# Optimization experiments

Measured on AMD Instinct MI355X. Metric: run time of the kernel, lower is better.

The kernel has to match this reference:

```python
import jax, jax.numpy as jnp
import numpy as np

B, T, D = 64, 2048, 256

def setup_inputs() -> dict:
    key = jax.random.key(0)
    k1, _ = jax.random.split(key)
    ts = jnp.arange(T, dtype=jnp.float32) * 0.01  # increasing time grid
    noise = jax.random.normal(k1, (B, T, D), dtype=jnp.float32)
    mu = jnp.zeros((D,), jnp.float32)
    log_kappa = jnp.full((D,), -0.7, jnp.float32)
    log_sigma = jnp.full((D,), -0.7, jnp.float32)
    return {"ts": ts, "noise": noise, "mu": mu, "log_kappa": log_kappa, "log_sigma": log_sigma}

def _A_Q(kappa, sigma, dt):
    # exact OU transition coefficients; dt: [T-1,1], kappa/sigma: [D] -> [T-1,D]
    A = jnp.exp(-kappa * dt)
    two_k_dt = 2.0 * kappa * dt
    small = (two_k_dt < 1e-6).astype(dt.dtype)
    Q_exact = sigma ** 2 * (1.0 - jnp.exp(-two_k_dt)) / jnp.maximum(2.0 * kappa, 1e-12)
    Q_taylor = sigma ** 2 * dt * (1.0 - kappa * dt + two_k_dt ** 2 / 6.0)
    Q = small * Q_taylor + (1.0 - small) * Q_exact
    return A, Q

def reference(ts, noise, mu, log_kappa, log_sigma):
    kappa = jax.nn.softplus(log_kappa) + 1e-6
    sigma = jax.nn.softplus(log_sigma) + 1e-6
    var0 = sigma ** 2 / (2.0 * kappa)                      # stationary variance [D]
    y0 = mu + noise[:, 0, :] * jnp.sqrt(var0)              # [B,D]
    dt = jnp.maximum(ts[1:] - ts[:-1], 1e-6)[:, None]      # [T-1,1]
    A, Q = _A_Q(kappa, sigma, dt)                          # [T-1,D]
    # mean = mu + A*(y-mu) = A*y + mu*(1-A); fold noise in ahead of the scan
    b = mu * (1.0 - A)                                     # [T-1,D]
    eps = jnp.swapaxes(noise[:, 1:, :], 0, 1) * jnp.sqrt(Q)[:, None, :]  # [T-1,B,D]

    def step(y, xs):
        A_k, b_k, e_k = xs
        y_new = A_k * y + b_k + e_k
        return y_new, y_new

    _, ys = jax.lax.scan(step, y0, (A, b, eps))            # [T-1,B,D]
    y = jnp.concatenate([y0[None], ys], axis=0)            # [T,B,D]
    return jnp.swapaxes(y, 0, 1)                           # [B,T,D]
```

## Files before the change

### kernel.cpp

```cpp
#include <hip/hip_runtime.h>
#include <math.h>

#define BB 64
#define TT 2048
#define DD 256
#define DP 128
#define SS 32
#define LL (TT / SS)


__device__ __forceinline__ float softplus_f(float x) {
    return (x > 0.f) ? (x + log1pf(expf(-x))) : log1pf(expf(x));
}

struct OUParams {
    float kx, ky;
    float s2x, s2y;
    float rx, ry;
    float mx, my;
};

__device__ __forceinline__ OUParams load_params(const float2* __restrict__ mu2,
                                                const float2* __restrict__ lk2,
                                                const float2* __restrict__ ls2,
                                                int tid) {
    float2 lk = lk2[tid], ls = ls2[tid], mu = mu2[tid];
    OUParams p;
    p.kx = softplus_f(lk.x) + 1e-6f;
    p.ky = softplus_f(lk.y) + 1e-6f;
    float sx = softplus_f(ls.x) + 1e-6f;
    float sy = softplus_f(ls.y) + 1e-6f;
    p.s2x = sx * sx;
    p.s2y = sy * sy;
    p.rx = p.s2x / fmaxf(2.f * p.kx, 1e-12f);
    p.ry = p.s2y / fmaxf(2.f * p.ky, 1e-12f);
    p.mx = mu.x;
    p.my = mu.y;
    return p;
}

__device__ __forceinline__ void ou_coeff(float dt, float kappa, float s2, float r,
                                         float mu, float& A, float& bm, float& sQ) {
    float e = kappa * dt;
    A = __expf(-e);
    float two = 2.f * e;
    float Qe = r * (1.f - A * A);
    float Qt = s2 * dt * fmaf(two * two, (1.f / 6.f), 1.f - e);
    float Q = (two < 1e-6f) ? Qt : Qe;
    sQ = sqrtf(Q);
    bm = mu * (1.f - A);
}

__global__ __launch_bounds__(128) void ou_pass1(
    const float* __restrict__ ts, const float2* __restrict__ noise2,
    const float2* __restrict__ mu2, const float2* __restrict__ lk2,
    const float2* __restrict__ ls2,
    float2* __restrict__ Pw, float2* __restrict__ Uw) {
    __shared__ float dts[LL];
    const int tid = threadIdx.x;
    const int s = blockIdx.x / BB;
    const int b = blockIdx.x % BB;
    const int t0 = s * LL;

    if (tid < LL) {
        int k = t0 + tid;
        float dt = 1e-6f;
        if (k >= 1) dt = fmaxf(ts[k] - ts[k - 1], 1e-6f);
        dts[tid] = dt;
    }
    __syncthreads();

    OUParams p = load_params(mu2, lk2, ls2, tid);
    const float2* np = noise2 + (size_t)b * TT * DP + tid;

    float2 U = {0.f, 0.f};
    float2 P = {1.f, 1.f};
    int kstart = t0;
    if (s == 0) {
        float2 n0 = np[0];
        U.x = fmaf(n0.x, sqrtf(p.rx), p.mx);
        U.y = fmaf(n0.y, sqrtf(p.ry), p.my);
        P.x = 0.f; P.y = 0.f;
        kstart = 1;
    }

#pragma unroll 4
    for (int k = kstart; k < t0 + LL; ++k) {
        float dt = dts[k - t0];
        float2 n = np[(size_t)k * DP];
        float Ax, bmx, sqx, Ay, bmy, sqy;
        ou_coeff(dt, p.kx, p.s2x, p.rx, p.mx, Ax, bmx, sqx);
        ou_coeff(dt, p.ky, p.s2y, p.ry, p.my, Ay, bmy, sqy);
        float cx = fmaf(sqx, n.x, bmx);
        float cy = fmaf(sqy, n.y, bmy);
        U.x = fmaf(Ax, U.x, cx);
        U.y = fmaf(Ay, U.y, cy);
        P.x *= Ax;
        P.y *= Ay;
    }

    size_t idx = ((size_t)s * BB + b) * DP + tid;
    Pw[idx] = P;
    Uw[idx] = U;
}

__global__ __launch_bounds__(128) void ou_pass2(
    const float2* __restrict__ Pw, const float2* __restrict__ Uw,
    float2* __restrict__ Ys) {
    const int tid = threadIdx.x;
    const int b = blockIdx.x;
    const size_t stride = (size_t)BB * DP;
    const size_t i0 = (size_t)b * DP + tid;

    float2 inc = Uw[i0];
    for (int s = 1; s < SS; ++s) {
        size_t idx = i0 + (size_t)s * stride;
        float2 Pv = Pw[idx];
        float2 Uv = Uw[idx];
        Ys[idx] = inc;
        inc.x = fmaf(Pv.x, inc.x, Uv.x);
        inc.y = fmaf(Pv.y, inc.y, Uv.y);
    }
}

__global__ __launch_bounds__(128) void ou_pass3(
    const float* __restrict__ ts, const float2* __restrict__ noise2,
    const float2* __restrict__ mu2, const float2* __restrict__ lk2,
    const float2* __restrict__ ls2,
    const float2* __restrict__ Ys, float2* __restrict__ out2) {
    __shared__ float dts[LL];
    const int tid = threadIdx.x;
    const int s = blockIdx.x / BB;
    const int b = blockIdx.x % BB;
    const int t0 = s * LL;

    if (tid < LL) {
        int k = t0 + tid;
        float dt = 1e-6f;
        if (k >= 1) dt = fmaxf(ts[k] - ts[k - 1], 1e-6f);
        dts[tid] = dt;
    }
    __syncthreads();

    OUParams p = load_params(mu2, lk2, ls2, tid);
    const float2* np = noise2 + (size_t)b * TT * DP + tid;
    float2* op = out2 + (size_t)b * TT * DP + tid;

    float2 y;
    int kstart = t0;
    if (s == 0) {
        float2 n0 = np[0];
        y.x = fmaf(n0.x, sqrtf(p.rx), p.mx);
        y.y = fmaf(n0.y, sqrtf(p.ry), p.my);
        op[0] = y;
        kstart = 1;
    } else {
        y = Ys[((size_t)s * BB + b) * DP + tid];
    }

#pragma unroll 4
    for (int k = kstart; k < t0 + LL; ++k) {
        float dt = dts[k - t0];
        float2 n = np[(size_t)k * DP];
        float Ax, bmx, sqx, Ay, bmy, sqy;
        ou_coeff(dt, p.kx, p.s2x, p.rx, p.mx, Ax, bmx, sqx);
        ou_coeff(dt, p.ky, p.s2y, p.ry, p.my, Ay, bmy, sqy);
        float cx = fmaf(sqx, n.x, bmx);
        float cy = fmaf(sqy, n.y, bmy);
        y.x = fmaf(Ax, y.x, cx);
        y.y = fmaf(Ay, y.y, cy);
        op[(size_t)k * DP] = y;
    }
}

__global__ __launch_bounds__(128) void ou_fallback(
    const float* __restrict__ ts, const float2* __restrict__ noise2,
    const float2* __restrict__ mu2, const float2* __restrict__ lk2,
    const float2* __restrict__ ls2, float2* __restrict__ out2) {
    __shared__ float dts[TT];
    const int tid = threadIdx.x;
    const int b = blockIdx.x;
    for (int i = tid; i < TT; i += 128) {
        float dt = 1e-6f;
        if (i >= 1) dt = fmaxf(ts[i] - ts[i - 1], 1e-6f);
        dts[i] = dt;
    }
    __syncthreads();

    OUParams p = load_params(mu2, lk2, ls2, tid);
    const float2* np = noise2 + (size_t)b * TT * DP + tid;
    float2* op = out2 + (size_t)b * TT * DP + tid;

    float2 n0 = np[0];
    float2 y;
    y.x = fmaf(n0.x, sqrtf(p.rx), p.mx);
    y.y = fmaf(n0.y, sqrtf(p.ry), p.my);
    op[0] = y;

#pragma unroll 4
    for (int k = 1; k < TT; ++k) {
        float dt = dts[k];
        float2 n = np[(size_t)k * DP];
        float Ax, bmx, sqx, Ay, bmy, sqy;
        ou_coeff(dt, p.kx, p.s2x, p.rx, p.mx, Ax, bmx, sqx);
        ou_coeff(dt, p.ky, p.s2y, p.ry, p.my, Ay, bmy, sqy);
        float cx = fmaf(sqx, n.x, bmx);
        float cy = fmaf(sqy, n.y, bmy);
        y.x = fmaf(Ax, y.x, cx);
        y.y = fmaf(Ay, y.y, cy);
        op[(size_t)k * DP] = y;
    }
}

extern "C" void kernel_launch(void* const* d_in, const int* in_sizes, int n_in,
                              void* d_out, int out_size, void* d_ws, size_t ws_size,
                              hipStream_t stream) {
    const float* ts = (const float*)d_in[0];
    const float2* noise2 = (const float2*)d_in[1];
    const float2* mu2 = (const float2*)d_in[2];
    const float2* lk2 = (const float2*)d_in[3];
    const float2* ls2 = (const float2*)d_in[4];
    float2* out2 = (float2*)d_out;

    const size_t seg = (size_t)SS * BB * DP;
    if (ws_size >= 3 * seg * sizeof(float2)) {
        float2* Pw = (float2*)d_ws;
        float2* Uw = Pw + seg;
        float2* Ys = Uw + seg;
        ou_pass1<<<SS * BB, 128, 0, stream>>>(ts, noise2, mu2, lk2, ls2, Pw, Uw);
        ou_pass2<<<BB, 128, 0, stream>>>(Pw, Uw, Ys);
        ou_pass3<<<SS * BB, 128, 0, stream>>>(ts, noise2, mu2, lk2, ls2, Ys, out2);
    } else {
        ou_fallback<<<BB, 128, 0, stream>>>(ts, noise2, mu2, lk2, ls2, out2);
    }
}
```

Measured before the change: 89.35 us.

## Vectorize OU scan to float4, cache coefficients per dt, nontemporal stores

Moves the three-pass chunked scan from float2 to float4 per thread, with one 64-lane wave per batch row and four rows per block. The chunk count rises from 32 to 64, and the per-step OU coefficients are recomputed only when dt changes. Output stores become nontemporal. The aim is wider memory transactions, fewer exp/sqrt per element and more parallel chunks. The cost is a longer serial pass2 and more register pressure from the float4 coefficient state.

Measured after the change: 90.52 us. No clear change (+1.3%).

```diff
diff --git a/kernel.cpp b/kernel.cpp
--- a/kernel.cpp
+++ b/kernel.cpp
@@ -4,172 +4,197 @@
 #define BB 64
 #define TT 2048
 #define DD 256
-#define DP 128
-#define SS 32
+#define D4 64
+#define SS 64
 #define LL (TT / SS)
+#define WPB 4
+#define BPG (BB / WPB)
+
+typedef float f4 __attribute__((ext_vector_type(4)));
 
 
 __device__ __forceinline__ float softplus_f(float x) {
     return (x > 0.f) ? (x + log1pf(expf(-x))) : log1pf(expf(x));
 }
 
-struct OUParams {
-    float kx, ky;
-    float s2x, s2y;
-    float rx, ry;
-    float mx, my;
-};
-
-__device__ __forceinline__ OUParams load_params(const float2* __restrict__ mu2,
-                                                const float2* __restrict__ lk2,
-                                                const float2* __restrict__ ls2,
-                                                int tid) {
-    float2 lk = lk2[tid], ls = ls2[tid], mu = mu2[tid];
-    OUParams p;
-    p.kx = softplus_f(lk.x) + 1e-6f;
-    p.ky = softplus_f(lk.y) + 1e-6f;
-    float sx = softplus_f(ls.x) + 1e-6f;
-    float sy = softplus_f(ls.y) + 1e-6f;
-    p.s2x = sx * sx;
-    p.s2y = sy * sy;
-    p.rx = p.s2x / fmaxf(2.f * p.kx, 1e-12f);
-    p.ry = p.s2y / fmaxf(2.f * p.ky, 1e-12f);
-    p.mx = mu.x;
-    p.my = mu.y;
+struct P4 { f4 k, s2, r, mu; };
+struct C4 { f4 A, bm, sQ; };
+struct P1 { float k, s2, r; };
+struct C1 { float A, bm, sQ; };
+
+__device__ __forceinline__ P1 sp1(float lk, float ls) {
+    P1 o;
+    o.k = softplus_f(lk) + 1e-6f;
+    float s = softplus_f(ls) + 1e-6f;
+    o.s2 = s * s;
+    o.r = o.s2 / fmaxf(2.f * o.k, 1e-12f);
+    return o;
+}
+
+__device__ __forceinline__ P4 load_params4(const f4* __restrict__ mu4,
+                                           const f4* __restrict__ lk4,
+                                           const f4* __restrict__ ls4,
+                                           int lane) {
+    f4 lk = lk4[lane], ls = ls4[lane], mu = mu4[lane];
+    P4 p;
+    P1 a;
+    a = sp1(lk.x, ls.x); p.k.x = a.k; p.s2.x = a.s2; p.r.x = a.r;
+    a = sp1(lk.y, ls.y); p.k.y = a.k; p.s2.y = a.s2; p.r.y = a.r;
+    a = sp1(lk.z, ls.z); p.k.z = a.k; p.s2.z = a.s2; p.r.z = a.r;
+    a = sp1(lk.w, ls.w); p.k.w = a.k; p.s2.w = a.s2; p.r.w = a.r;
+    p.mu = mu;
     return p;
 }
 
-__device__ __forceinline__ void ou_coeff(float dt, float kappa, float s2, float r,
-                                         float mu, float& A, float& bm, float& sQ) {
+__device__ __forceinline__ C1 ou_coeff(float dt, float kappa, float s2, float r,
+                                       float mu) {
+    C1 o;
     float e = kappa * dt;
-    A = __expf(-e);
+    o.A = __expf(-e);
     float two = 2.f * e;
-    float Qe = r * (1.f - A * A);
+    float Qe = r * (1.f - o.A * o.A);
     float Qt = s2 * dt * fmaf(two * two, (1.f / 6.f), 1.f - e);
     float Q = (two < 1e-6f) ? Qt : Qe;
-    sQ = sqrtf(Q);
-    bm = mu * (1.f - A);
-}
-
-__global__ __launch_bounds__(128) void ou_pass1(
-    const float* __restrict__ ts, const float2* __restrict__ noise2,
-    const float2* __restrict__ mu2, const float2* __restrict__ lk2,
-    const float2* __restrict__ ls2,
-    float2* __restrict__ Pw, float2* __restrict__ Uw) {
+    o.sQ = sqrtf(Q);
+    o.bm = mu * (1.f - o.A);
+    return o;
+}
+
+__device__ __forceinline__ C4 coeff4(float dt, const P4& p) {
+    C4 c;
+    C1 o;
+    o = ou_coeff(dt, p.k.x, p.s2.x, p.r.x, p.mu.x); c.A.x = o.A; c.bm.x = o.bm; c.sQ.x = o.sQ;
+    o = ou_coeff(dt, p.k.y, p.s2.y, p.r.y, p.mu.y); c.A.y = o.A; c.bm.y = o.bm; c.sQ.y = o.sQ;
+    o = ou_coeff(dt, p.k.z, p.s2.z, p.r.z, p.mu.z); c.A.z = o.A; c.bm.z = o.bm; c.sQ.z = o.sQ;
+    o = ou_coeff(dt, p.k.w, p.s2.w, p.r.w, p.mu.w); c.A.w = o.A; c.bm.w = o.bm; c.sQ.w = o.sQ;
+    return c;
+}
+
+__device__ __forceinline__ void ou_step4(const C4& cc, const f4 n, f4& y) {
+    f4 cv = cc.sQ * n + cc.bm;
+    y = cc.A * y + cv;
+}
+
+__device__ __forceinline__ f4 sqrt4(const f4 v) {
+    f4 r;
+    r.x = sqrtf(v.x); r.y = sqrtf(v.y); r.z = sqrtf(v.z); r.w = sqrtf(v.w);
+    return r;
+}
+
+__global__ __launch_bounds__(256) void ou_pass1(
+    const float* __restrict__ ts, const f4* __restrict__ noise4,
+    const f4* __restrict__ mu4, const f4* __restrict__ lk4,
+    const f4* __restrict__ ls4,
+    f4* __restrict__ Pw, f4* __restrict__ Uw) {
     __shared__ float dts[LL];
-    const int tid = threadIdx.x;
-    const int s = blockIdx.x / BB;
-    const int b = blockIdx.x % BB;
+    const int lane = threadIdx.x & 63;
+    const int w = threadIdx.x >> 6;
+    const int s = blockIdx.x / BPG;
+    const int bg = blockIdx.x % BPG;
+    const int b = bg * WPB + w;
     const int t0 = s * LL;
 
-    if (tid < LL) {
-        int k = t0 + tid;
+    if (threadIdx.x < LL) {
+        int k = t0 + threadIdx.x;
         float dt = 1e-6f;
         if (k >= 1) dt = fmaxf(ts[k] - ts[k - 1], 1e-6f);
-        dts[tid] = dt;
+        dts[threadIdx.x] = dt;
     }
     __syncthreads();
 
-    OUParams p = load_params(mu2, lk2, ls2, tid);
-    const float2* np = noise2 + (size_t)b * TT * DP + tid;
-
-    float2 U = {0.f, 0.f};
-    float2 P = {1.f, 1.f};
+    P4 p = load_params4(mu4, lk4, ls4, lane);
+    const f4* np = noise4 + (size_t)b * TT * D4 + lane;
+
+    f4 U = {0.f, 0.f, 0.f, 0.f};
+    f4 P = {1.f, 1.f, 1.f, 1.f};
     int kstart = t0;
     if (s == 0) {
-        float2 n0 = np[0];
-        U.x = fmaf(n0.x, sqrtf(p.rx), p.mx);
-        U.y = fmaf(n0.y, sqrtf(p.ry), p.my);
-        P.x = 0.f; P.y = 0.f;
+        f4 n0 = np[0];
+        U = n0 * sqrt4(p.r) + p.mu;
+        P = (f4){0.f, 0.f, 0.f, 0.f};
         kstart = 1;
     }
 
+    float dtprev = -1.f;
+    C4 cc;
 #pragma unroll 4
     for (int k = kstart; k < t0 + LL; ++k) {
         float dt = dts[k - t0];
-        float2 n = np[(size_t)k * DP];
-        float Ax, bmx, sqx, Ay, bmy, sqy;
-        ou_coeff(dt, p.kx, p.s2x, p.rx, p.mx, Ax, bmx, sqx);
-        ou_coeff(dt, p.ky, p.s2y, p.ry, p.my, Ay, bmy, sqy);
-        float cx = fmaf(sqx, n.x, bmx);
-        float cy = fmaf(sqy, n.y, bmy);
-        U.x = fmaf(Ax, U.x, cx);
-        U.y = fmaf(Ay, U.y, cy);
-        P.x *= Ax;
-        P.y *= Ay;
-    }
-
-    size_t idx = ((size_t)s * BB + b) * DP + tid;
+        f4 n = np[(size_t)k * D4];
+        if (dt != dtprev) { cc = coeff4(dt, p); dtprev = dt; }
+        ou_step4(cc, n, U);
+        P *= cc.A;
+    }
+
+    size_t idx = ((size_t)s * BB + b) * D4 + lane;
     Pw[idx] = P;
     Uw[idx] = U;
 }
 
-__global__ __launch_bounds__(128) void ou_pass2(
-    const float2* __restrict__ Pw, const float2* __restrict__ Uw,
-    float2* __restrict__ Ys) {
-    const int tid = threadIdx.x;
+__global__ __launch_bounds__(64) void ou_pass2(
+    const f4* __restrict__ Pw, const f4* __restrict__ Uw,
+    f4* __restrict__ Ys) {
+    const int lane = threadIdx.x;
     const int b = blockIdx.x;
-    const size_t stride = (size_t)BB * DP;
-    const size_t i0 = (size_t)b * DP + tid;
-
-    float2 inc = Uw[i0];
+    const size_t stride = (size_t)BB * D4;
+    const size_t i0 = (size_t)b * D4 + lane;
+
+    f4 inc = Uw[i0];
+#pragma unroll 8
     for (int s = 1; s < SS; ++s) {
         size_t idx = i0 + (size_t)s * stride;
-        float2 Pv = Pw[idx];
-        float2 Uv = Uw[idx];
+        f4 Pv = Pw[idx];
+        f4 Uv = Uw[idx];
         Ys[idx] = inc;
-        inc.x = fmaf(Pv.x, inc.x, Uv.x);
-        inc.y = fmaf(Pv.y, inc.y, Uv.y);
-    }
-}
-
-__global__ __launch_bounds__(128) void ou_pass3(
-    const float* __restrict__ ts, const float2* __restrict__ noise2,
-    const float2* __restrict__ mu2, const float2* __restrict__ lk2,
-    const float2* __restrict__ ls2,
-    const float2* __restrict__ Ys, float2* __restrict__ out2) {
+        inc = Pv * inc + Uv;
+    }
+}
+
+__global__ __launch_bounds__(256) void ou_pass3(
+    const float* __restrict__ ts, const f4* __restrict__ noise4,
+    const f4* __restrict__ mu4, const f4* __restrict__ lk4,
+    const f4* __restrict__ ls4,
+    const f4* __restrict__ Ys, f4* __restrict__ out4) {
     __shared__ float dts[LL];
-    const int tid = threadIdx.x;
-    const int s = blockIdx.x / BB;
-    const int b = blockIdx.x % BB;
+    const int lane = threadIdx.x & 63;
+    const int w = threadIdx.x >> 6;
+    const int s = blockIdx.x / BPG;
+    const int bg = blockIdx.x % BPG;
+    const int b = bg * WPB + w;
     const int t0 = s * LL;
 
-    if (tid < LL) {
-        int k = t0 + tid;
+    if (threadIdx.x < LL) {
+        int k = t0 + threadIdx.x;
         float dt = 1e-6f;
         if (k >= 1) dt = fmaxf(ts[k] - ts[k - 1], 1e-6f);
-        dts[tid] = dt;
+        dts[threadIdx.x] = dt;
     }
     __syncthreads();
 
-    OUParams p = load_params(mu2, lk2, ls2, tid);
-    const float2* np = noise2 + (size_t)b * TT * DP + tid;
-    float2* op = out2 + (size_t)b * TT * DP + tid;
-
-    float2 y;
+    P4 p = load_params4(mu4, lk4, ls4, lane);
+    const f4* np = noise4 + (size_t)b * TT * D4 + lane;
+    f4* op = out4 + (size_t)b * TT * D4 + lane;
+
+    f4 y;
     int kstart = t0;
     if (s == 0) {
-        float2 n0 = np[0];
-        y.x = fmaf(n0.x, sqrtf(p.rx), p.mx);
-        y.y = fmaf(n0.y, sqrtf(p.ry), p.my);
-        op[0] = y;
+        f4 n0 = np[0];
+        y = n0 * sqrt4(p.r) + p.mu;
+        __builtin_nontemporal_store(y, op);
         kstart = 1;
     } else {
-        y = Ys[((size_t)s * BB + b) * DP + tid];
-    }
-
+        y = Ys[((size_t)s * BB + b) * D4 + lane];
+    }
+
+    float dtprev = -1.f;
+    C4 cc;
 #pragma unroll 4
     for (int k = kstart; k < t0 + LL; ++k) {
         float dt = dts[k - t0];
-        float2 n = np[(size_t)k * DP];
-        float Ax, bmx, sqx, Ay, bmy, sqy;
-        ou_coeff(dt, p.kx, p.s2x, p.rx, p.mx, Ax, bmx, sqx);
-        ou_coeff(dt, p.ky, p.s2y, p.ry, p.my, Ay, bmy, sqy);
-        float cx = fmaf(sqx, n.x, bmx);
-        float cy = fmaf(sqy, n.y, bmy);
-        y.x = fmaf(Ax, y.x, cx);
-        y.y = fmaf(Ay, y.y, cy);
-        op[(size_t)k * DP] = y;
+        f4 n = np[(size_t)k * D4];
+        if (dt != dtprev) { cc = coeff4(dt, p); dtprev = dt; }
+        ou_step4(cc, n, y);
+        __builtin_nontemporal_store(y, op + (size_t)k * D4);
     }
 }
 
@@ -187,28 +212,28 @@
     }
     __syncthreads();
 
-    OUParams p = load_params(mu2, lk2, ls2, tid);
-    const float2* np = noise2 + (size_t)b * TT * DP + tid;
-    float2* op = out2 + (size_t)b * TT * DP + tid;
+    float2 lk = lk2[tid], ls = ls2[tid], mu = mu2[tid];
+    P1 px = sp1(lk.x, ls.x);
+    P1 py = sp1(lk.y, ls.y);
+
+    const float2* np = noise2 + (size_t)b * TT * 128 + tid;
+    float2* op = out2 + (size_t)b * TT * 128 + tid;
 
     float2 n0 = np[0];
     float2 y;
-    y.x = fmaf(n0.x, sqrtf(p.rx), p.mx);
-    y.y = fmaf(n0.y, sqrtf(p.ry), p.my);
+    y.x = fmaf(n0.x, sqrtf(px.r), mu.x);
+    y.y = fmaf(n0.y, sqrtf(py.r), mu.y);
     op[0] = y;
 
 #pragma unroll 4
     for (int k = 1; k < TT; ++k) {
         float dt = dts[k];
-        float2 n = np[(size_t)k * DP];
-        float Ax, bmx, sqx, Ay, bmy, sqy;
-        ou_coeff(dt, p.kx, p.s2x, p.rx, p.mx, Ax, bmx, sqx);
-        ou_coeff(dt, p.ky, p.s2y, p.ry, p.my, Ay, bmy, sqy);
-        float cx = fmaf(sqx, n.x, bmx);
-        float cy = fmaf(sqy, n.y, bmy);
-        y.x = fmaf(Ax, y.x, cx);
-        y.y = fmaf(Ay, y.y, cy);
-        op[(size_t)k * DP] = y;
+        float2 n = np[(size_t)k * 128];
+        C1 cx = ou_coeff(dt, px.k, px.s2, px.r, mu.x);
+        C1 cy = ou_coeff(dt, py.k, py.s2, py.r, mu.y);
+        y.x = fmaf(cx.A, y.x, fmaf(cx.sQ, n.x, cx.bm));
+        y.y = fmaf(cy.A, y.y, fmaf(cy.sQ, n.y, cy.bm));
+        op[(size_t)k * 128] = y;
     }
 }
 
@@ -216,21 +241,25 @@
                               void* d_out, int out_size, void* d_ws, size_t ws_size,
                               hipStream_t stream) {
     const float* ts = (const float*)d_in[0];
-    const float2* noise2 = (const float2*)d_in[1];
-    const float2* mu2 = (const float2*)d_in[2];
-    const float2* lk2 = (const float2*)d_in[3];
-    const float2* ls2 = (const float2*)d_in[4];
-    float2* out2 = (float2*)d_out;
-
-    const size_t seg = (size_t)SS * BB * DP;
-    if (ws_size >= 3 * seg * sizeof(float2)) {
-        float2* Pw = (float2*)d_ws;
-        float2* Uw = Pw + seg;
-        float2* Ys = Uw + seg;
-        ou_pass1<<<SS * BB, 128, 0, stream>>>(ts, noise2, mu2, lk2, ls2, Pw, Uw);
-        ou_pass2<<<BB, 128, 0, stream>>>(Pw, Uw, Ys);
-        ou_pass3<<<SS * BB, 128, 0, stream>>>(ts, noise2, mu2, lk2, ls2, Ys, out2);
+    const f4* noise4 = (const f4*)d_in[1];
+    const f4* mu4 = (const f4*)d_in[2];
+    const f4* lk4 = (const f4*)d_in[3];
+    const f4* ls4 = (const f4*)d_in[4];
+    f4* out4 = (f4*)d_out;
+
+    const size_t seg = (size_t)SS * BB * D4;
+    if (ws_size >= 3 * seg * sizeof(f4)) {
+        f4* Pw = (f4*)d_ws;
+        f4* Uw = Pw + seg;
+        f4* Ys = Uw + seg;
+        ou_pass1<<<SS * BPG, 256, 0, stream>>>(ts, noise4, mu4, lk4, ls4, Pw, Uw);
+        ou_pass2<<<BB, 64, 0, stream>>>(Pw, Uw, Ys);
+        ou_pass3<<<SS * BPG, 256, 0, stream>>>(ts, noise4, mu4, lk4, ls4, Ys, out4);
     } else {
-        ou_fallback<<<BB, 128, 0, stream>>>(ts, noise2, mu2, lk2, ls2, out2);
-    }
-}
+        ou_fallback<<<BB, 128, 0, stream>>>(ts, (const float2*)d_in[1],
+                                            (const float2*)d_in[2],
+                                            (const float2*)d_in[3],
+                                            (const float2*)d_in[4],
+                                            (float2*)d_out);
+    }
+}
```
